# Kernel tuning notes

Hardware: AMD Instinct MI355X
Metric: run time of the kernel (lower is better)

## Reference

```python
import jax, jax.numpy as jnp
import numpy as np
from jax import lax


def _median_blur(img, k):
    # img: [B, H, W]; k odd (3 here). Replicate border like cv2.medianBlur.
    p = k // 2
    B, H, W = img.shape
    xp = jnp.pad(img, ((0, 0), (p, p), (p, p)), mode='edge')
    # Gather the k*k shifted views -> [B, H, W, k*k]
    wins = jnp.stack([xp[:, i:i + H, j:j + W] for i in range(k) for j in range(k)], axis=-1)
    return jnp.median(wins, axis=-1)


def setup_inputs() -> dict:
    key = jax.random.key(0)
    kx, kt = jax.random.split(key)
    x = jax.random.normal(kx, (32, 1, 512, 512), dtype=jnp.float32)
    t_tensor = jax.random.randint(kt, (32,), 0, 10).astype(jnp.int64)
    return {"x": x, "t_tensor": t_tensor, "kernel_size": 3, "num_timesteps": 10}


def reference(x, t_tensor, kernel_size, num_timesteps):
    # Faithful vectorized version of MedianBlur.forward_process:
    # sample i gets t_tensor[i] successive median blurs.
    B, C, H, W = x.shape  # C == 1, matching the .squeeze() in the original
    img = x[:, 0, :, :]  # [B, H, W]
    t = t_tensor.astype(jnp.int32)

    def step(cur, j):
        blurred = _median_blur(cur, kernel_size)
        active = (j < t)[:, None, None]  # only samples with t_i > j keep blurring
        return jnp.where(active, blurred, cur), None

    out, _ = lax.scan(step, img, jnp.arange(num_timesteps, dtype=jnp.int32))
    return out[:, None, :, :]  # restore channel dim, like unsqueeze(0) per sample
```

## Files before the change

### kernel.cpp

```cpp
#include <hip/hip_runtime.h>


#define TD 50
#define OW 32
#define P  6
#define RAD 9
#define NT 64

__device__ __forceinline__ float min3f(float a, float b, float c) { return fminf(fminf(a, b), c); }
__device__ __forceinline__ float max3f(float a, float b, float c) { return fmaxf(fmaxf(a, b), c); }
__device__ __forceinline__ float med3f(float a, float b, float c) { return __builtin_amdgcn_fmed3f(a, b, c); }

__global__ __launch_bounds__(NT, 4) void median_fused_kernel(
    const float* __restrict__ src, float* __restrict__ dst,
    const int* __restrict__ t)
{
    __shared__ float buf[TD * TD];

    const int b   = blockIdx.y;
    const int ty  = blockIdx.x >> 4;
    const int tx  = blockIdx.x & 15;
    const int y0  = ty * OW;
    const int x0  = tx * OW;
    const int tid = threadIdx.x;
    const float* img  = src + (b << 18);
    float*       outb = dst + (b << 18);

    int T = t[b];
    T = min(max(T, 0), 9);

    if (T == 0) {
        for (int idx = tid; idx < 256; idx += NT) {
            int row = idx >> 3, c4 = idx & 7;
            *(float4*)&outb[((y0 + row) << 9) + x0 + (c4 << 2)] =
                *(const float4*)&img[((y0 + row) << 9) + x0 + (c4 << 2)];
        }
        return;
    }

    for (int i = tid; i < TD * TD; i += NT) {
        int r = i / TD, c = i - r * TD;
        int gy = min(max(y0 - RAD + r, 0), 511);
        int gx = min(max(x0 - RAD + c, 0), 511);
        buf[i] = img[(gy << 9) + gx];
    }

    const int ptx = tid & 7;
    const int pty = tid >> 3;
    const int ub  = 1 + P * pty;
    const int vb  = 1 + P * ptx;

    const bool padTop = (y0 == 0)   && (pty == 1);
    const bool padBot = (y0 == 480) && (pty == 6);
    const bool padLft = (x0 == 0)   && (ptx == 1);
    const bool padRgt = (x0 == 480) && (ptx == 6);

    __syncthreads();

    float stage[36];
    #pragma unroll
    for (int i = 0; i < 6; ++i)
        #pragma unroll
        for (int j = 0; j < 6; ++j)
            stage[i * 6 + j] = buf[(ub + i) * TD + vb + j];

    for (int k = 0; k < T; ++k) {
        float A[8], Br[8], C[8];
        {
            const float* p = &buf[(ub - 1) * TD + (vb - 1)];
            #pragma unroll
            for (int j = 0; j < 8; ++j) A[j] = p[j];
        }
        Br[0] = buf[ub * TD + (vb - 1)];
        #pragma unroll
        for (int j = 0; j < 6; ++j) Br[1 + j] = stage[j];
        Br[7] = buf[ub * TD + (vb + 6)];

        #pragma unroll
        for (int i = 0; i < 6; ++i) {
            if (i < 5) {
                C[0] = buf[(ub + 1 + i) * TD + (vb - 1)];
                #pragma unroll
                for (int j = 0; j < 6; ++j) C[1 + j] = stage[(i + 1) * 6 + j];
                C[7] = buf[(ub + 1 + i) * TD + (vb + 6)];
            } else {
                const float* p = &buf[(ub + 6) * TD + (vb - 1)];
                #pragma unroll
                for (int j = 0; j < 8; ++j) C[j] = p[j];
            }
            float lo[8], mi[8], hi[8];
            #pragma unroll
            for (int j = 0; j < 8; ++j) {
                lo[j] = min3f(A[j], Br[j], C[j]);
                mi[j] = med3f(A[j], Br[j], C[j]);
                hi[j] = max3f(A[j], Br[j], C[j]);
            }
            #pragma unroll
            for (int j = 0; j < 6; ++j)
                stage[i * 6 + j] = med3f(max3f(lo[j], lo[j+1], lo[j+2]),
                                         med3f(mi[j], mi[j+1], mi[j+2]),
                                         min3f(hi[j], hi[j+1], hi[j+2]));
            #pragma unroll
            for (int j = 0; j < 8; ++j) { A[j] = Br[j]; Br[j] = C[j]; }
        }

        if (padTop) {
            #pragma unroll
            for (int j = 0; j < 6; ++j) stage[6 + j] = stage[12 + j];
        }
        if (padBot) {
            #pragma unroll
            for (int j = 0; j < 6; ++j) stage[24 + j] = stage[18 + j];
        }
        if (padLft) {
            #pragma unroll
            for (int i = 0; i < 6; ++i) stage[i * 6 + 1] = stage[i * 6 + 2];
        }
        if (padRgt) {
            #pragma unroll
            for (int i = 0; i < 6; ++i) stage[i * 6 + 4] = stage[i * 6 + 3];
        }

        __syncthreads();

        if (k == T - 1) {
            #pragma unroll
            for (int i = 0; i < 6; ++i)
                #pragma unroll
                for (int j = 0; j < 6; ++j)
                    buf[(ub + i) * TD + vb + j] = stage[i * 6 + j];
        } else {
            #pragma unroll
            for (int j = 0; j < 6; ++j) {
                buf[ub * TD + vb + j]       = stage[j];
                buf[(ub + 5) * TD + vb + j] = stage[30 + j];
            }
            #pragma unroll
            for (int i = 1; i < 5; ++i) {
                buf[(ub + i) * TD + vb]     = stage[i * 6];
                buf[(ub + i) * TD + vb + 5] = stage[i * 6 + 5];
            }
        }

        __syncthreads();
    }

    for (int idx = tid; idx < 256; idx += NT) {
        int row = idx >> 3, c4 = idx & 7;
        const float* s = &buf[(RAD + row) * TD + RAD + (c4 << 2)];
        float4 v = { s[0], s[1], s[2], s[3] };
        *(float4*)&outb[((y0 + row) << 9) + x0 + (c4 << 2)] = v;
    }
}

extern "C" void kernel_launch(void* const* d_in, const int* in_sizes, int n_in,
                              void* d_out, int out_size, void* d_ws, size_t ws_size,
                              hipStream_t stream) {
    const float* x   = (const float*)d_in[0];
    const int*   t   = (const int*)d_in[1];
    float*       out = (float*)d_out;

    dim3 block(NT);
    dim3 grid(256, 32);
    median_fused_kernel<<<grid, block, 0, stream>>>(x, out, t);
}
```

Measured before the change: 117.2 us.

## Exchange tile halos via wavefront shuffles instead of LDS and barriers

Each thread's 6x6 register tile now gets its neighbour halo through cross-lane shuffles (__shfl_up/__shfl_down) inside the 64-lane wavefront. The per-iteration LDS stores, loads and two __syncthreads barriers go away. Outer-ring halo values for edge threads are loaded once from LDS before the loop and kept in registers. The median network is written out as an explicit macro, and the launch-bounds occupancy hint is removed, which may raise register use and shuffle traffic.

New measurement: 117.4 us. Within noise of the previous version (+0.2%).

```diff
diff --git a/kernel.cpp b/kernel.cpp
--- a/kernel.cpp
+++ b/kernel.cpp
@@ -1,17 +1,34 @@
 #include <hip/hip_runtime.h>
 
 
-#define TD 50
-#define OW 32
-#define P  6
+#define TD  50
+#define OW  32
 #define RAD 9
-#define NT 64
-
-__device__ __forceinline__ float min3f(float a, float b, float c) { return fminf(fminf(a, b), c); }
-__device__ __forceinline__ float max3f(float a, float b, float c) { return fmaxf(fmaxf(a, b), c); }
-__device__ __forceinline__ float med3f(float a, float b, float c) { return __builtin_amdgcn_fmed3f(a, b, c); }
-
-__global__ __launch_bounds__(NT, 4) void median_fused_kernel(
+#define NT  64
+
+static __device__ __forceinline__ float min3f(float a, float b, float c) { return fminf(fminf(a, b), c); }
+static __device__ __forceinline__ float max3f(float a, float b, float c) { return fmaxf(fmaxf(a, b), c); }
+static __device__ __forceinline__ float med3f(float a, float b, float c) { return __builtin_amdgcn_fmed3f(a, b, c); }
+
+#define MEDSTEP(O0,O1,O2,O3,O4,O5) { \
+    float lo0=min3f(A0,B0,C0), mi0=med3f(A0,B0,C0), hi0=max3f(A0,B0,C0); \
+    float lo1=min3f(A1,B1,C1), mi1=med3f(A1,B1,C1), hi1=max3f(A1,B1,C1); \
+    float lo2=min3f(A2,B2,C2), mi2=med3f(A2,B2,C2), hi2=max3f(A2,B2,C2); \
+    float lo3=min3f(A3,B3,C3), mi3=med3f(A3,B3,C3), hi3=max3f(A3,B3,C3); \
+    float lo4=min3f(A4,B4,C4), mi4=med3f(A4,B4,C4), hi4=max3f(A4,B4,C4); \
+    float lo5=min3f(A5,B5,C5), mi5=med3f(A5,B5,C5), hi5=max3f(A5,B5,C5); \
+    float lo6=min3f(A6,B6,C6), mi6=med3f(A6,B6,C6), hi6=max3f(A6,B6,C6); \
+    float lo7=min3f(A7,B7,C7), mi7=med3f(A7,B7,C7), hi7=max3f(A7,B7,C7); \
+    O0 = med3f(max3f(lo0,lo1,lo2), med3f(mi0,mi1,mi2), min3f(hi0,hi1,hi2)); \
+    O1 = med3f(max3f(lo1,lo2,lo3), med3f(mi1,mi2,mi3), min3f(hi1,hi2,hi3)); \
+    O2 = med3f(max3f(lo2,lo3,lo4), med3f(mi2,mi3,mi4), min3f(hi2,hi3,hi4)); \
+    O3 = med3f(max3f(lo3,lo4,lo5), med3f(mi3,mi4,mi5), min3f(hi3,hi4,hi5)); \
+    O4 = med3f(max3f(lo4,lo5,lo6), med3f(mi4,mi5,mi6), min3f(hi4,hi5,hi6)); \
+    O5 = med3f(max3f(lo5,lo6,lo7), med3f(mi5,mi6,mi7), min3f(hi5,hi6,hi7)); \
+    A0=B0;A1=B1;A2=B2;A3=B3;A4=B4;A5=B5;A6=B6;A7=B7; \
+    B0=C0;B1=C1;B2=C2;B3=C3;B4=C4;B5=C5;B6=C6;B7=C7; }
+
+__global__ __launch_bounds__(NT) void median_fused_kernel(
     const float* __restrict__ src, float* __restrict__ dst,
     const int* __restrict__ t)
 {
@@ -47,8 +64,11 @@
 
     const int ptx = tid & 7;
     const int pty = tid >> 3;
-    const int ub  = 1 + P * pty;
-    const int vb  = 1 + P * ptx;
+    const int ub  = 1 + 6 * pty;
+    const int vb  = 1 + 6 * ptx;
+
+    const bool topB = (pty == 0), botB = (pty == 7);
+    const bool lftB = (ptx == 0), rgtB = (ptx == 7);
 
     const bool padTop = (y0 == 0)   && (pty == 1);
     const bool padBot = (y0 == 480) && (pty == 6);
@@ -57,6 +77,16 @@
 
     __syncthreads();
 
+    float topA[8], botC[8], lftL[8], rgtR[8];
+    #pragma unroll
+    for (int j = 0; j < 8; ++j) topA[j] = topB ? buf[0 * TD + (vb - 1 + j)] : 0.f;
+    #pragma unroll
+    for (int j = 0; j < 8; ++j) botC[j] = botB ? buf[49 * TD + (vb - 1 + j)] : 0.f;
+    #pragma unroll
+    for (int i = 0; i < 8; ++i) lftL[i] = lftB ? buf[(ub - 1 + i) * TD + 0] : 0.f;
+    #pragma unroll
+    for (int i = 0; i < 8; ++i) rgtR[i] = rgtB ? buf[(ub - 1 + i) * TD + 49] : 0.f;
+
     float stage[36];
     #pragma unroll
     for (int i = 0; i < 6; ++i)
@@ -65,85 +95,89 @@
             stage[i * 6 + j] = buf[(ub + i) * TD + vb + j];
 
     for (int k = 0; k < T; ++k) {
-        float A[8], Br[8], C[8];
-        {
-            const float* p = &buf[(ub - 1) * TD + (vb - 1)];
-            #pragma unroll
-            for (int j = 0; j < 8; ++j) A[j] = p[j];
-        }
-        Br[0] = buf[ub * TD + (vb - 1)];
+        float a1 = __shfl_up(stage[30], 8), a2 = __shfl_up(stage[31], 8);
+        float a3 = __shfl_up(stage[32], 8), a4 = __shfl_up(stage[33], 8);
+        float a5 = __shfl_up(stage[34], 8), a6 = __shfl_up(stage[35], 8);
+        float aul = __shfl_up(stage[35], 9);
+        float aur = __shfl_up(stage[30], 7);
+        float d1 = __shfl_down(stage[0], 8), d2 = __shfl_down(stage[1], 8);
+        float d3 = __shfl_down(stage[2], 8), d4 = __shfl_down(stage[3], 8);
+        float d5 = __shfl_down(stage[4], 8), d6 = __shfl_down(stage[5], 8);
+        float ddl = __shfl_down(stage[5], 7);
+        float ddr = __shfl_down(stage[0], 9);
+        float l0 = __shfl_up(stage[5], 1),  l1 = __shfl_up(stage[11], 1);
+        float l2 = __shfl_up(stage[17], 1), l3 = __shfl_up(stage[23], 1);
+        float l4 = __shfl_up(stage[29], 1), l5 = __shfl_up(stage[35], 1);
+        float r0 = __shfl_down(stage[0], 1),  r1 = __shfl_down(stage[6], 1);
+        float r2 = __shfl_down(stage[12], 1), r3 = __shfl_down(stage[18], 1);
+        float r4 = __shfl_down(stage[24], 1), r5 = __shfl_down(stage[30], 1);
+
+        float A0 = topB ? topA[0] : (lftB ? lftL[0] : aul);
+        float A1 = topB ? topA[1] : a1;
+        float A2 = topB ? topA[2] : a2;
+        float A3 = topB ? topA[3] : a3;
+        float A4 = topB ? topA[4] : a4;
+        float A5 = topB ? topA[5] : a5;
+        float A6 = topB ? topA[6] : a6;
+        float A7 = topB ? topA[7] : (rgtB ? rgtR[0] : aur);
+
+        float Dn0 = botB ? botC[0] : (lftB ? lftL[7] : ddl);
+        float Dn1 = botB ? botC[1] : d1;
+        float Dn2 = botB ? botC[2] : d2;
+        float Dn3 = botB ? botC[3] : d3;
+        float Dn4 = botB ? botC[4] : d4;
+        float Dn5 = botB ? botC[5] : d5;
+        float Dn6 = botB ? botC[6] : d6;
+        float Dn7 = botB ? botC[7] : (rgtB ? rgtR[7] : ddr);
+
+        float Lc0 = lftB ? lftL[1] : l0, Lc1 = lftB ? lftL[2] : l1;
+        float Lc2 = lftB ? lftL[3] : l2, Lc3 = lftB ? lftL[4] : l3;
+        float Lc4 = lftB ? lftL[5] : l4, Lc5 = lftB ? lftL[6] : l5;
+        float Rc0 = rgtB ? rgtR[1] : r0, Rc1 = rgtB ? rgtR[2] : r1;
+        float Rc2 = rgtB ? rgtR[3] : r2, Rc3 = rgtB ? rgtR[4] : r3;
+        float Rc4 = rgtB ? rgtR[5] : r4, Rc5 = rgtB ? rgtR[6] : r5;
+
+        float B0 = Lc0, B1 = stage[0], B2 = stage[1], B3 = stage[2],
+              B4 = stage[3], B5 = stage[4], B6 = stage[5], B7 = Rc0;
+        float C0, C1, C2, C3, C4, C5, C6, C7;
+
+        C0=Lc1; C1=stage[6];  C2=stage[7];  C3=stage[8];  C4=stage[9];  C5=stage[10]; C6=stage[11]; C7=Rc1;
+        MEDSTEP(stage[0],stage[1],stage[2],stage[3],stage[4],stage[5])
+        C0=Lc2; C1=stage[12]; C2=stage[13]; C3=stage[14]; C4=stage[15]; C5=stage[16]; C6=stage[17]; C7=Rc2;
+        MEDSTEP(stage[6],stage[7],stage[8],stage[9],stage[10],stage[11])
+        C0=Lc3; C1=stage[18]; C2=stage[19]; C3=stage[20]; C4=stage[21]; C5=stage[22]; C6=stage[23]; C7=Rc3;
+        MEDSTEP(stage[12],stage[13],stage[14],stage[15],stage[16],stage[17])
+        C0=Lc4; C1=stage[24]; C2=stage[25]; C3=stage[26]; C4=stage[27]; C5=stage[28]; C6=stage[29]; C7=Rc4;
+        MEDSTEP(stage[18],stage[19],stage[20],stage[21],stage[22],stage[23])
+        C0=Lc5; C1=stage[30]; C2=stage[31]; C3=stage[32]; C4=stage[33]; C5=stage[34]; C6=stage[35]; C7=Rc5;
+        MEDSTEP(stage[24],stage[25],stage[26],stage[27],stage[28],stage[29])
+        C0=Dn0; C1=Dn1; C2=Dn2; C3=Dn3; C4=Dn4; C5=Dn5; C6=Dn6; C7=Dn7;
+        MEDSTEP(stage[30],stage[31],stage[32],stage[33],stage[34],stage[35])
+
+        if (padTop) {
+            #pragma unroll
+            for (int j = 0; j < 6; ++j) stage[6 + j] = stage[12 + j];
+        }
+        if (padBot) {
+            #pragma unroll
+            for (int j = 0; j < 6; ++j) stage[24 + j] = stage[18 + j];
+        }
+        if (padLft) {
+            #pragma unroll
+            for (int i = 0; i < 6; ++i) stage[i * 6 + 1] = stage[i * 6 + 2];
+        }
+        if (padRgt) {
+            #pragma unroll
+            for (int i = 0; i < 6; ++i) stage[i * 6 + 4] = stage[i * 6 + 3];
+        }
+    }
+
+    #pragma unroll
+    for (int i = 0; i < 6; ++i)
         #pragma unroll
-        for (int j = 0; j < 6; ++j) Br[1 + j] = stage[j];
-        Br[7] = buf[ub * TD + (vb + 6)];
-
-        #pragma unroll
-        for (int i = 0; i < 6; ++i) {
-            if (i < 5) {
-                C[0] = buf[(ub + 1 + i) * TD + (vb - 1)];
-                #pragma unroll
-                for (int j = 0; j < 6; ++j) C[1 + j] = stage[(i + 1) * 6 + j];
-                C[7] = buf[(ub + 1 + i) * TD + (vb + 6)];
-            } else {
-                const float* p = &buf[(ub + 6) * TD + (vb - 1)];
-                #pragma unroll
-                for (int j = 0; j < 8; ++j) C[j] = p[j];
-            }
-            float lo[8], mi[8], hi[8];
-            #pragma unroll
-            for (int j = 0; j < 8; ++j) {
-                lo[j] = min3f(A[j], Br[j], C[j]);
-                mi[j] = med3f(A[j], Br[j], C[j]);
-                hi[j] = max3f(A[j], Br[j], C[j]);
-            }
-            #pragma unroll
-            for (int j = 0; j < 6; ++j)
-                stage[i * 6 + j] = med3f(max3f(lo[j], lo[j+1], lo[j+2]),
-                                         med3f(mi[j], mi[j+1], mi[j+2]),
-                                         min3f(hi[j], hi[j+1], hi[j+2]));
-            #pragma unroll
-            for (int j = 0; j < 8; ++j) { A[j] = Br[j]; Br[j] = C[j]; }
-        }
-
-        if (padTop) {
-            #pragma unroll
-            for (int j = 0; j < 6; ++j) stage[6 + j] = stage[12 + j];
-        }
-        if (padBot) {
-            #pragma unroll
-            for (int j = 0; j < 6; ++j) stage[24 + j] = stage[18 + j];
-        }
-        if (padLft) {
-            #pragma unroll
-            for (int i = 0; i < 6; ++i) stage[i * 6 + 1] = stage[i * 6 + 2];
-        }
-        if (padRgt) {
-            #pragma unroll
-            for (int i = 0; i < 6; ++i) stage[i * 6 + 4] = stage[i * 6 + 3];
-        }
-
-        __syncthreads();
-
-        if (k == T - 1) {
-            #pragma unroll
-            for (int i = 0; i < 6; ++i)
-                #pragma unroll
-                for (int j = 0; j < 6; ++j)
-                    buf[(ub + i) * TD + vb + j] = stage[i * 6 + j];
-        } else {
-            #pragma unroll
-            for (int j = 0; j < 6; ++j) {
-                buf[ub * TD + vb + j]       = stage[j];
-                buf[(ub + 5) * TD + vb + j] = stage[30 + j];
-            }
-            #pragma unroll
-            for (int i = 1; i < 5; ++i) {
-                buf[(ub + i) * TD + vb]     = stage[i * 6];
-                buf[(ub + i) * TD + vb + 5] = stage[i * 6 + 5];
-            }
-        }
-
-        __syncthreads();
-    }
+        for (int j = 0; j < 6; ++j)
+            buf[(ub + i) * TD + vb + j] = stage[i * 6 + j];
+    __syncthreads();
 
     for (int idx = tid; idx < 256; idx += NT) {
         int row = idx >> 3, c4 = idx & 7;
```
